# Optimization experiments

Measured on AMD Instinct MI355X. Metric: run time of the kernel, lower is better.

## Reference

```python
import jax, jax.numpy as jnp
import numpy as np

B, F, BOND, NFREQ, NOUT, INIT_STD = 16384, 256, 16, 4, 1, 0.1


def setup_inputs() -> dict:
    key = jax.random.key(0)
    ks = jax.random.split(key, 10)
    x = jax.random.uniform(ks[0], (B, F), dtype=jnp.float32)
    inp = {"x": x, "frequency_min": jnp.array(1.0, dtype=jnp.float32)}
    d_in = 1 + 2 * NFREQ  # physical leg dim = 9
    n, level = F, 0
    while n > 1:
        n2 = n // 2
        d_out = NOUT if n == 2 else BOND
        # stack all same-level node tensors: [n_pairs, d_left, d_right, d_out]
        inp[f"W{level}"] = jax.random.normal(ks[level + 1], (n2, d_in, d_in, d_out), dtype=jnp.float32) * INIT_STD
        d_in, n, level = d_out, n2, level + 1
    return inp


def reference(x, frequency_min, W0, W1, W2, W3, W4, W5, W6, W7):
    Ws = [W0, W1, W2, W3, W4, W5, W6, W7]
    nfreq = (W0.shape[1] - 1) // 2
    # Fourier feature map: [B, F, 1+2*nfreq]
    xs = (x * frequency_min)[..., None]
    freqs = jnp.arange(1, nfreq + 1, dtype=x.dtype)
    feats = jnp.concatenate(
        [jnp.ones_like(xs), jnp.sin(xs * freqs), jnp.cos(xs * freqs)], axis=-1
    )
    nodes = feats  # [B, n_nodes, d]
    for W in Ws:
        left = nodes[:, 0::2]   # [B, n/2, d]
        right = nodes[:, 1::2]  # [B, n/2, d]
        # batched pairwise bilinear contraction over all nodes of one level
        nodes = jnp.einsum('bni,nijd,bnj->bnd', left, W, right)
    return nodes[:, 0, :]  # [B, NOUT]
```

## Files before the change

### kernel.cpp

```cpp
#include <hip/hip_runtime.h>
#include <math.h>

#define BTOT 16384

typedef __attribute__((ext_vector_type(8))) short s16x8;
typedef __attribute__((ext_vector_type(4))) float f32x4;
typedef __attribute__((ext_vector_type(4))) uint u32x4;
typedef __attribute__((ext_vector_type(2))) float f32x2;
typedef __attribute__((ext_vector_type(2))) uint u32x2;

#define OFF0 0u
#define OFF1 655360u
#define OFF2 1179648u
#define OFF3 1441792u
#define OFF4 1572864u
#define OFF5 1638400u
#define OFF6 1671168u
#define OFF7 1687552u

__device__ __forceinline__ ushort rtn_bf16(float x) {
  uint u = __builtin_bit_cast(uint, x);
  uint r = u + 0x7fffu + ((u >> 16) & 1u);
  return (ushort)(r >> 16);
}

__global__ __launch_bounds__(256) void wprep_kernel(
    const float* __restrict__ W0, const float* __restrict__ W1,
    const float* __restrict__ W2, const float* __restrict__ W3,
    const float* __restrict__ W4, const float* __restrict__ W5,
    const float* __restrict__ W6, const float* __restrict__ W7,
    ushort* __restrict__ U) {
  __shared__ float WL[4096];
  int blk = blockIdx.x;
  const float* Wsrc; ushort* dst; int ktN, din, nsrc; bool dout1 = false;
  if (blk < 128)      { Wsrc = W0 + blk * 1296;         dst = U + OFF0 + (size_t)blk * 5120;         ktN = 5; din = 9;  nsrc = 1296; }
  else if (blk < 192) { Wsrc = W1 + (blk - 128) * 4096; dst = U + OFF1 + (size_t)(blk - 128) * 8192; ktN = 8; din = 16; nsrc = 4096; }
  else if (blk < 224) { Wsrc = W2 + (blk - 192) * 4096; dst = U + OFF2 + (size_t)(blk - 192) * 8192; ktN = 8; din = 16; nsrc = 4096; }
  else if (blk < 240) { Wsrc = W3 + (blk - 224) * 4096; dst = U + OFF3 + (size_t)(blk - 224) * 8192; ktN = 8; din = 16; nsrc = 4096; }
  else if (blk < 248) { Wsrc = W4 + (blk - 240) * 4096; dst = U + OFF4 + (size_t)(blk - 240) * 8192; ktN = 8; din = 16; nsrc = 4096; }
  else if (blk < 252) { Wsrc = W5 + (blk - 248) * 4096; dst = U + OFF5 + (size_t)(blk - 248) * 8192; ktN = 8; din = 16; nsrc = 4096; }
  else if (blk < 254) { Wsrc = W6 + (blk - 252) * 4096; dst = U + OFF6 + (size_t)(blk - 252) * 8192; ktN = 8; din = 16; nsrc = 4096; }
  else                { Wsrc = W7;                      dst = U + OFF7;                              ktN = 8; din = 16; nsrc = 256; dout1 = true; }
  for (int i = threadIdx.x; i < nsrc; i += 256) WL[i] = Wsrc[i];
  __syncthreads();
  int entries = ktN * 512;
  for (int e = threadIdx.x; e < entries; e += 256) {
    int kt = e >> 9, l = (e >> 3) & 63, jv = e & 7;
    int k = kt * 32 + ((l >> 4) << 3) + jv;
    int i = k >> 4, j = k & 15, n = l & 15;
    float w;
    if (dout1) w = (n == 0) ? WL[i * 16 + j] : 0.f;
    else       w = (i < din && j < din) ? WL[(i * din + j) * 16 + n] : 0.f;
    uint u = __builtin_bit_cast(uint, w);
    uint h = u & 0xffff0000u;
    dst[e] = (ushort)(h >> 16);
    dst[entries + e] = rtn_bf16(w - __builtin_bit_cast(float, h));
  }
}

__device__ __forceinline__ f32x4 split3(float li, const f32x2* rf2,
                                        s16x8 wh, s16x8 wl, f32x4 acc) {
  const f32x2 li2 = {li, li};
  u32x4 hv, lv;
#pragma unroll
  for (int jp = 0; jp < 4; ++jp) {
    f32x2 p2 = li2 * rf2[jp];
    u32x2 u2 = __builtin_bit_cast(u32x2, p2);
    u32x2 hb = u2 & 0xffff0000u;
    f32x2 h2 = __builtin_bit_cast(f32x2, hb);
    f32x2 q2 = __builtin_elementwise_fma(li2, rf2[jp], -h2);
    u32x2 uq = __builtin_bit_cast(u32x2, q2);
    hv[jp] = __builtin_amdgcn_perm(u2.y, u2.x, 0x07060302u);
    lv[jp] = __builtin_amdgcn_perm(uq.y, uq.x, 0x07060302u);
  }
  s16x8 ahi = __builtin_bit_cast(s16x8, hv);
  s16x8 alo = __builtin_bit_cast(s16x8, lv);
  acc = __builtin_amdgcn_mfma_f32_16x16x32_bf16(ahi, wh, acc, 0, 0, 0);
  acc = __builtin_amdgcn_mfma_f32_16x16x32_bf16(alo, wh, acc, 0, 0, 0);
  acc = __builtin_amdgcn_mfma_f32_16x16x32_bf16(ahi, wl, acc, 0, 0, 0);
  return acc;
}

template <int KTN, bool L0M>
__device__ __forceinline__ f32x4 mfma_core(const float* Lcol, const float* Rcol,
                                           const int ld, const ushort* __restrict__ Wf,
                                           int lane) {
  const int g = lane >> 4;
  const int j0 = (g & 1) * 8, gh = g >> 1;
  const float* Lg = Lcol + gh * ld;
  float lf[KTN];
#pragma unroll
  for (int i = 0; i < KTN; ++i)
    lf[i] = (L0M && (2 * i + gh > 8)) ? 0.f : Lg[2 * i * ld];
  f32x2 rf2[4];
#pragma unroll
  for (int j = 0; j < 8; ++j) {
    float v = (L0M && (j0 + j >= 9)) ? 0.f : Rcol[(j0 + j) * ld];
    rf2[j >> 1][j & 1] = v;
  }
  f32x4 acc = {0.f, 0.f, 0.f, 0.f};
  const int entries = KTN * 512;
#pragma unroll
  for (int kt = 0; kt < KTN; ++kt) {
    const s16x8 wh = *(const s16x8*)&Wf[(kt * 64 + lane) * 8];
    const s16x8 wl = *(const s16x8*)&Wf[entries + (kt * 64 + lane) * 8];
    acc = split3(lf[kt], rf2, wh, wl, acc);
  }
  return acc;
}

#define LDF 67

__device__ __forceinline__ void feats_col(float xv, float* Fb, int col) {
  float s1 = __sinf(xv), c1 = __cosf(xv);
  Fb[0 * LDF + col] = 1.f; Fb[1 * LDF + col] = s1; Fb[5 * LDF + col] = c1;
  float sk = s1, ck = c1;
#pragma unroll
  for (int k = 2; k <= 4; ++k) {
    float sn = s1 * ck + c1 * sk, cn = c1 * ck - s1 * sk;
    sk = sn; ck = cn;
    Fb[k * LDF + col] = sk; Fb[(4 + k) * LDF + col] = ck;
  }
}

__global__ __launch_bounds__(256, 4) void ttn_front_kernel(
    const float* __restrict__ x, const float* __restrict__ fminp,
    const ushort* __restrict__ U, float* __restrict__ s1out) {
  __shared__ float F0[9 * LDF], F1[9 * LDF];
  __shared__ float A0[16 * LDF], B0[16 * LDF];
  __shared__ float A1[16 * LDF], B1[16 * LDF];
  __shared__ float A2[16 * LDF], B2[16 * LDF];

  const int tid = threadIdx.x;
  const int lane = tid & 63, w = tid >> 6;
  const int m = lane & 15, g = lane >> 4;
  const int bl = w * 16 + m;
  const int b0 = blockIdx.x * 64;
  const int s = blockIdx.y;
  const float fmin = fminp[0];

  const float* xw = x + (size_t)(b0 + w * 16 + (lane & 15)) * 256 + s * 16;
  float* outG = s1out + (size_t)(s * 16) * BTOT + b0;

  auto storeL = [&](f32x4 a, float* Out) {
#pragma unroll
    for (int r = 0; r < 4; ++r) Out[m * LDF + w * 16 + g * 4 + r] = a[r];
  };

  for (int t = 0; t < 8; ++t) {
    if (lane < 32) {
      int side = lane >> 4;
      float xv = xw[2 * t + side] * fmin;
      feats_col(xv, side ? F1 : F0, w * 16 + (lane & 15));
    }
    f32x4 a = mfma_core<5, true>(&F0[bl], &F1[bl], LDF,
                                 U + OFF0 + (size_t)(8 * s + t) * 5120, lane);
    storeL(a, (t & 1) ? B0 : A0);
    if (t & 1) {
      f32x4 c1 = mfma_core<8, false>(&A0[bl], &B0[bl], LDF,
                                     U + OFF1 + (size_t)(4 * s + (t >> 1)) * 8192, lane);
      storeL(c1, ((t >> 1) & 1) ? B1 : A1);
      if ((t & 3) == 3) {
        f32x4 c2 = mfma_core<8, false>(&A1[bl], &B1[bl], LDF,
                                       U + OFF2 + (size_t)(2 * s + (t >> 2)) * 8192, lane);
        storeL(c2, ((t >> 2) & 1) ? B2 : A2);
        if (t == 7) {
          f32x4 c3 = mfma_core<8, false>(&A2[bl], &B2[bl], LDF,
                                         U + OFF3 + (size_t)s * 8192, lane);
#pragma unroll
          for (int r = 0; r < 4; ++r)
            outG[(size_t)m * BTOT + w * 16 + g * 4 + r] = c3[r];
        }
      }
    }
  }
}

__global__ __launch_bounds__(512) void ttn_back_kernel(
    const float* __restrict__ s1, const ushort* __restrict__ U,
    float* __restrict__ out) {
  __shared__ float T[256 * 17];
  __shared__ float P[8][16 * 17];
  const int tid = threadIdx.x;
  const int lane = tid & 63, v = tid >> 6;
  const int m = lane & 15, g = lane >> 4;
  const int b0 = blockIdx.x * 16;

  auto storeC = [&](f32x4 a, float* Buf) {
#pragma unroll
    for (int r = 0; r < 4; ++r) Buf[m * 17 + g * 4 + r] = a[r];
  };

#pragma unroll
  for (int it = 0; it < 2; ++it) {
    int idx = it * 512 + tid;
    int r = idx >> 2, c4 = (idx & 3) * 4;
    float4 vv = *(const float4*)&s1[(size_t)r * BTOT + b0 + c4];
    T[r * 17 + c4 + 0] = vv.x; T[r * 17 + c4 + 1] = vv.y;
    T[r * 17 + c4 + 2] = vv.z; T[r * 17 + c4 + 3] = vv.w;
  }
  __syncthreads();

  {
    f32x4 a = mfma_core<8, false>(&T[(32 * v) * 17 + m], &T[(32 * v + 16) * 17 + m],
                                  17, U + OFF4 + (size_t)v * 8192, lane);
    storeC(a, P[v]);
  }
  __syncthreads();

  if (v < 4) {
    f32x4 a = mfma_core<8, false>(&P[2 * v][m], &P[2 * v + 1][m], 17,
                                  U + OFF5 + (size_t)v * 8192, lane);
    storeC(a, &T[v * 16 * 17]);
  }
  __syncthreads();

  if (v < 2) {
    f32x4 a = mfma_core<8, false>(&T[(2 * v) * 16 * 17 + m],
                                  &T[(2 * v + 1) * 16 * 17 + m], 17,
                                  U + OFF6 + (size_t)v * 8192, lane);
    storeC(a, P[v]);
  }
  __syncthreads();

  if (v == 0) {
    f32x4 a = mfma_core<8, false>(&P[0][m], &P[1][m], 17, U + OFF7, lane);
    if (m == 0) {
#pragma unroll
      for (int r = 0; r < 4; ++r) out[b0 + g * 4 + r] = a[r];
    }
  }
}

extern "C" void kernel_launch(void* const* d_in, const int* in_sizes, int n_in,
                              void* d_out, int out_size, void* d_ws, size_t ws_size,
                              hipStream_t stream) {
  const float* x    = (const float*)d_in[0];
  const float* fmin = (const float*)d_in[1];
  const float* W0   = (const float*)d_in[2];
  const float* W1   = (const float*)d_in[3];
  const float* W2   = (const float*)d_in[4];
  const float* W3   = (const float*)d_in[5];
  const float* W4   = (const float*)d_in[6];
  const float* W5   = (const float*)d_in[7];
  const float* W6   = (const float*)d_in[8];
  const float* W7   = (const float*)d_in[9];
  float* out = (float*)d_out;

  ushort* U = (ushort*)d_ws;
  float* s1 = (float*)((char*)d_ws + (4u << 20));

  wprep_kernel<<<255, 256, 0, stream>>>(W0, W1, W2, W3, W4, W5, W6, W7, U);
  ttn_front_kernel<<<dim3(256, 16), 256, 0, stream>>>(x, fmin, U, s1);
  ttn_back_kernel<<<1024, 512, 0, stream>>>(s1, U, out);
}
```

Before: 234.6 us.

## Fuse back tree levels into front kernel via last-block atomic counter

```diff
diff --git a/kernel.cpp b/kernel.cpp
--- a/kernel.cpp
+++ b/kernel.cpp
@@ -29,9 +29,10 @@
     const float* __restrict__ W2, const float* __restrict__ W3,
     const float* __restrict__ W4, const float* __restrict__ W5,
     const float* __restrict__ W6, const float* __restrict__ W7,
-    ushort* __restrict__ U) {
+    ushort* __restrict__ U, uint* __restrict__ cnt) {
   __shared__ float WL[4096];
   int blk = blockIdx.x;
+  if (blk == 0) cnt[threadIdx.x] = 0;
   const float* Wsrc; ushort* dst; int ktN, din, nsrc; bool dout1 = false;
   if (blk < 128)      { Wsrc = W0 + blk * 1296;         dst = U + OFF0 + (size_t)blk * 5120;         ktN = 5; din = 9;  nsrc = 1296; }
   else if (blk < 192) { Wsrc = W1 + (blk - 128) * 4096; dst = U + OFF1 + (size_t)(blk - 128) * 8192; ktN = 8; din = 16; nsrc = 4096; }
@@ -123,19 +124,23 @@
   }
 }
 
-__global__ __launch_bounds__(256, 4) void ttn_front_kernel(
+__global__ __launch_bounds__(256, 4) void ttn_fused_kernel(
     const float* __restrict__ x, const float* __restrict__ fminp,
-    const ushort* __restrict__ U, float* __restrict__ s1out) {
-  __shared__ float F0[9 * LDF], F1[9 * LDF];
-  __shared__ float A0[16 * LDF], B0[16 * LDF];
-  __shared__ float A1[16 * LDF], B1[16 * LDF];
-  __shared__ float A2[16 * LDF], B2[16 * LDF];
+    const ushort* __restrict__ U, float* __restrict__ s1out,
+    uint* __restrict__ cnt, float* __restrict__ out) {
+  __shared__ float LB[7638];
+  __shared__ int isLastS;
+  float* F0 = LB;            float* F1 = LB + 603;
+  float* A0 = LB + 1206;     float* B0 = LB + 2278;
+  float* A1 = LB + 3350;     float* B1 = LB + 4422;
+  float* A2 = LB + 5494;     float* B2 = LB + 6566;
 
   const int tid = threadIdx.x;
   const int lane = tid & 63, w = tid >> 6;
   const int m = lane & 15, g = lane >> 4;
   const int bl = w * 16 + m;
-  const int b0 = blockIdx.x * 64;
+  const int bblk = blockIdx.x;
+  const int b0 = bblk * 64;
   const int s = blockIdx.y;
   const float fmin = fminp[0];
 
@@ -174,61 +179,46 @@
       }
     }
   }
-}
-
-__global__ __launch_bounds__(512) void ttn_back_kernel(
-    const float* __restrict__ s1, const ushort* __restrict__ U,
-    float* __restrict__ out) {
-  __shared__ float T[256 * 17];
-  __shared__ float P[8][16 * 17];
-  const int tid = threadIdx.x;
-  const int lane = tid & 63, v = tid >> 6;
-  const int m = lane & 15, g = lane >> 4;
-  const int b0 = blockIdx.x * 16;
-
+
+  __threadfence();
+  __syncthreads();
+  if (tid == 0) isLastS = (atomicAdd(&cnt[bblk], 1u) == 15u);
+  __syncthreads();
+  if (!isLastS) return;
+  __threadfence();
+
+  const float* s1r = s1out + b0 + 16 * w;
+  float* P0 = LB + w * 1632;
+  float* P1 = P0 + 272;
+  float* Q  = P0 + 544;
   auto storeC = [&](f32x4 a, float* Buf) {
 #pragma unroll
     for (int r = 0; r < 4; ++r) Buf[m * 17 + g * 4 + r] = a[r];
   };
 
 #pragma unroll
-  for (int it = 0; it < 2; ++it) {
-    int idx = it * 512 + tid;
-    int r = idx >> 2, c4 = (idx & 3) * 4;
-    float4 vv = *(const float4*)&s1[(size_t)r * BTOT + b0 + c4];
-    T[r * 17 + c4 + 0] = vv.x; T[r * 17 + c4 + 1] = vv.y;
-    T[r * 17 + c4 + 2] = vv.z; T[r * 17 + c4 + 3] = vv.w;
-  }
-  __syncthreads();
-
-  {
-    f32x4 a = mfma_core<8, false>(&T[(32 * v) * 17 + m], &T[(32 * v + 16) * 17 + m],
-                                  17, U + OFF4 + (size_t)v * 8192, lane);
-    storeC(a, P[v]);
-  }
-  __syncthreads();
-
-  if (v < 4) {
-    f32x4 a = mfma_core<8, false>(&P[2 * v][m], &P[2 * v + 1][m], 17,
-                                  U + OFF5 + (size_t)v * 8192, lane);
-    storeC(a, &T[v * 16 * 17]);
-  }
-  __syncthreads();
-
-  if (v < 2) {
-    f32x4 a = mfma_core<8, false>(&T[(2 * v) * 16 * 17 + m],
-                                  &T[(2 * v + 1) * 16 * 17 + m], 17,
-                                  U + OFF6 + (size_t)v * 8192, lane);
-    storeC(a, P[v]);
-  }
-  __syncthreads();
-
-  if (v == 0) {
-    f32x4 a = mfma_core<8, false>(&P[0][m], &P[1][m], 17, U + OFF7, lane);
-    if (m == 0) {
-#pragma unroll
-      for (int r = 0; r < 4; ++r) out[b0 + g * 4 + r] = a[r];
-    }
+  for (int h = 0; h < 4; ++h) {
+    f32x4 a0 = mfma_core<8, false>(&s1r[(size_t)(64 * h) * BTOT + m],
+                                   &s1r[(size_t)(64 * h + 16) * BTOT + m],
+                                   BTOT, U + OFF4 + (size_t)(2 * h) * 8192, lane);
+    storeC(a0, P0);
+    f32x4 a1 = mfma_core<8, false>(&s1r[(size_t)(64 * h + 32) * BTOT + m],
+                                   &s1r[(size_t)(64 * h + 48) * BTOT + m],
+                                   BTOT, U + OFF4 + (size_t)(2 * h + 1) * 8192, lane);
+    storeC(a1, P1);
+    f32x4 a5 = mfma_core<8, false>(&P0[m], &P1[m], 17,
+                                   U + OFF5 + (size_t)h * 8192, lane);
+    storeC(a5, Q + h * 272);
+  }
+  f32x4 a60 = mfma_core<8, false>(&Q[m], &Q[272 + m], 17, U + OFF6, lane);
+  storeC(a60, P0);
+  f32x4 a61 = mfma_core<8, false>(&Q[544 + m], &Q[816 + m], 17,
+                                  U + OFF6 + 8192, lane);
+  storeC(a61, P1);
+  f32x4 a7 = mfma_core<8, false>(&P0[m], &P1[m], 17, U + OFF7, lane);
+  if (m == 0) {
+#pragma unroll
+    for (int r = 0; r < 4; ++r) out[b0 + 16 * w + g * 4 + r] = a7[r];
   }
 }
 
@@ -249,8 +239,8 @@
 
   ushort* U = (ushort*)d_ws;
   float* s1 = (float*)((char*)d_ws + (4u << 20));
-
-  wprep_kernel<<<255, 256, 0, stream>>>(W0, W1, W2, W3, W4, W5, W6, W7, U);
-  ttn_front_kernel<<<dim3(256, 16), 256, 0, stream>>>(x, fmin, U, s1);
-  ttn_back_kernel<<<1024, 512, 0, stream>>>(s1, U, out);
-}
+  uint* cnt = (uint*)((char*)d_ws + (4u << 20) + (size_t)16 * 16 * BTOT * 4);
+
+  wprep_kernel<<<255, 256, 0, stream>>>(W0, W1, W2, W3, W4, W5, W6, W7, U, cnt);
+  ttn_fused_kernel<<<dim3(256, 16), 256, 0, stream>>>(x, fmin, U, s1, cnt, out);
+}
```

New measurement: 613.3 us. +161.4%, slower.
